# Optimization experiments

Hardware: AMD Instinct MI355X
Metric: run time of the kernel (lower is better)

Reference implementation:

```python
import jax, jax.numpy as jnp
import numpy as np

EPS = 1e-5
PDIM, QKD, DIM = 64, 16, 256
SCALE = QKD ** -0.5


def setup_inputs() -> dict:
    key = jax.random.key(0)
    ks = jax.random.split(key, 13)
    B, H, W = 8, 64, 64
    return {
        "x": jax.random.normal(ks[0], (B, DIM, H, W), jnp.float32),
        "gn_g": jax.random.uniform(ks[1], (PDIM,), jnp.float32, 0.5, 1.5),
        "gn_b": jax.random.normal(ks[2], (PDIM,), jnp.float32) * 0.1,
        "qkv_w": jax.random.normal(ks[3], (2 * QKD + PDIM, PDIM), jnp.float32) * (PDIM ** -0.5),
        "qkv_bn_g": jax.random.uniform(ks[4], (2 * QKD + PDIM,), jnp.float32, 0.5, 1.5),
        "qkv_bn_b": jax.random.normal(ks[5], (2 * QKD + PDIM,), jnp.float32) * 0.1,
        "qkv_rm": jax.random.normal(ks[6], (2 * QKD + PDIM,), jnp.float32) * 0.1,
        "qkv_rv": jax.random.uniform(ks[7], (2 * QKD + PDIM,), jnp.float32, 0.5, 1.5),
        "proj_w": jax.random.normal(ks[8], (DIM, DIM), jnp.float32) * (DIM ** -0.5),
        "proj_bn_g": jax.random.uniform(ks[9], (DIM,), jnp.float32, 0.5, 1.5),
        "proj_bn_b": jax.random.normal(ks[10], (DIM,), jnp.float32) * 0.1,
        "proj_rm": jax.random.normal(ks[11], (DIM,), jnp.float32) * 0.1,
        "proj_rv": jax.random.uniform(ks[12], (DIM,), jnp.float32, 0.5, 1.5),
    }


def _bn(y, g, b, rm, rv):
    # inference BatchNorm over channel axis 1 of [B,C,H,W]
    inv = g / jnp.sqrt(rv + EPS)
    return y * inv[None, :, None, None] + (b - rm * inv)[None, :, None, None]


def reference(x, gn_g, gn_b, qkv_w, qkv_bn_g, qkv_bn_b, qkv_rm, qkv_rv,
              proj_w, proj_bn_g, proj_bn_b, proj_rm, proj_rv):
    B, C, H, W = x.shape
    x1, x2 = x[:, :PDIM], x[:, PDIM:]
    # GroupNorm with 1 group: normalize over (C,H,W) per sample
    mu = jnp.mean(x1, axis=(1, 2, 3), keepdims=True)
    var = jnp.var(x1, axis=(1, 2, 3), keepdims=True)
    x1n = (x1 - mu) / jnp.sqrt(var + EPS)
    x1n = x1n * gn_g[None, :, None, None] + gn_b[None, :, None, None]
    # qkv: 1x1 conv + BN
    qkv = jnp.einsum('bchw,oc->bohw', x1n, qkv_w)
    qkv = _bn(qkv, qkv_bn_g, qkv_bn_b, qkv_rm, qkv_rv)
    q, k, v = qkv[:, :QKD], qkv[:, QKD:2 * QKD], qkv[:, 2 * QKD:]
    N = H * W
    q = q.reshape(B, QKD, N)
    k = k.reshape(B, QKD, N)
    v = v.reshape(B, PDIM, N)
    attn = jnp.einsum('bcn,bcm->bnm', q, k) * SCALE  # [B,N,N]
    attn = jax.nn.softmax(attn, axis=-1)
    x1_attn = jnp.einsum('bcm,bnm->bcn', v, attn).reshape(B, PDIM, H, W)
    xc = jnp.concatenate([x1_attn, x2], axis=1)
    # proj: ReLU -> 1x1 conv -> BN
    y = jnp.einsum('bchw,oc->bohw', jax.nn.relu(xc), proj_w)
    return _bn(y, proj_bn_g, proj_bn_b, proj_rm, proj_rv)
```

## Files before the change

### kernel.cpp

```cpp
#include <hip/hip_runtime.h>
#include <hip/hip_bf16.h>

typedef __bf16 bf16;
typedef __bf16 bf16x4 __attribute__((ext_vector_type(4)));
typedef __bf16 bf16x8 __attribute__((ext_vector_type(8)));
typedef float  f32x16 __attribute__((ext_vector_type(16)));

#define MFMA32 __builtin_amdgcn_mfma_f32_32x32x16_bf16
#define EPSV 1e-5f
#define QSCALE 0.36067376022224085f

__device__ __forceinline__ f32x16 fzero16() {
  f32x16 z;
#pragma unroll
  for (int i = 0; i < 16; ++i) z[i] = 0.f;
  return z;
}

__global__ __launch_bounds__(256) void k_stats_partial(const float* __restrict__ x,
                                                       float* __restrict__ part) {
  const int b = blockIdx.x >> 5, k = blockIdx.x & 31;
  const float* p = x + (size_t)b * 256 * 4096 + k * 8192;
  const int t = threadIdx.x;
  float s = 0.f, q = 0.f;
#pragma unroll
  for (int j = 0; j < 8; ++j) {
    float4 v = ((const float4*)p)[t + j * 256];
    s += v.x + v.y + v.z + v.w;
    q += v.x * v.x + v.y * v.y + v.z * v.z + v.w * v.w;
  }
  __shared__ float ls[256], lq[256];
  ls[t] = s; lq[t] = q;
  __syncthreads();
  for (int off = 128; off > 0; off >>= 1) {
    if (t < off) { ls[t] += ls[t + off]; lq[t] += lq[t + off]; }
    __syncthreads();
  }
  if (t == 0) { part[blockIdx.x * 2] = ls[0]; part[blockIdx.x * 2 + 1] = lq[0]; }
}

__global__ __launch_bounds__(256) void k_stats_final(const float* __restrict__ part,
                                                     float* __restrict__ stats) {
  const int t = threadIdx.x, b = t >> 5, k = t & 31;
  float s = part[(b * 32 + k) * 2], q = part[(b * 32 + k) * 2 + 1];
  for (int off = 16; off > 0; off >>= 1) {
    s += __shfl_down(s, off, 32);
    q += __shfl_down(q, off, 32);
  }
  if (k == 0) {
    const float inv_n = 1.f / 262144.f;
    const float mu = s * inv_n;
    const float var = q * inv_n - mu * mu;
    stats[b * 2] = mu;
    stats[b * 2 + 1] = rsqrtf(var + EPSV);
  }
}

__global__ __launch_bounds__(256) void k_qkv(
    const float* __restrict__ x, const float* __restrict__ gn_g, const float* __restrict__ gn_b,
    const float* __restrict__ qkv_w, const float* __restrict__ bn_g, const float* __restrict__ bn_b,
    const float* __restrict__ bn_rm, const float* __restrict__ bn_rv,
    const float* __restrict__ stats,
    bf16* __restrict__ qw, bf16* __restrict__ kw, bf16* __restrict__ vw) {
  const int b = blockIdx.x >> 6, tile = blockIdx.x & 63;
  const int n0 = tile * 64, t = threadIdx.x;
  __shared__ float xn[64][68];
  __shared__ float W[64][96];
  __shared__ float beta_s[96];
  const float mu = stats[b * 2], rstd = stats[b * 2 + 1];
  {
    const int c = t >> 2, f = t & 3;
    const float A = rstd * gn_g[c], B = gn_b[c] - mu * A;
    const float* xr = x + ((size_t)b * 256 + c) * 4096 + n0;
#pragma unroll
    for (int j = 0; j < 4; ++j) {
      float4 v = ((const float4*)xr)[f * 4 + j];
      const int nb = f * 16 + j * 4;
      xn[c][nb + 0] = v.x * A + B; xn[c][nb + 1] = v.y * A + B;
      xn[c][nb + 2] = v.z * A + B; xn[c][nb + 3] = v.w * A + B;
    }
  }
  for (int oc = t; oc < 96 * 8; oc += 256) {
    const int o = oc >> 3, ch = (oc & 7) * 8;
    const float inv = bn_g[o] * rsqrtf(bn_rv[o] + EPSV);
    if (ch == 0) beta_s[o] = bn_b[o] - bn_rm[o] * inv;
    const float* wr = qkv_w + o * 64 + ch;
#pragma unroll
    for (int i = 0; i < 8; ++i) W[ch + i][o] = wr[i] * inv;
  }
  __syncthreads();
  const int o_l = t & 31, ng = t >> 5;
#pragma unroll 1
  for (int p = 0; p < 3; ++p) {
    const int o = p * 32 + o_l;
    float acc[8];
#pragma unroll
    for (int j = 0; j < 8; ++j) acc[j] = 0.f;
    for (int c = 0; c < 64; ++c) {
      const float wv = W[c][o];
      const float* xr = &xn[c][ng * 8];
#pragma unroll
      for (int j = 0; j < 8; ++j) acc[j] += wv * xr[j];
    }
    const float beta = beta_s[o];
    const int nb = n0 + ng * 8;
    if (p == 0) {
      if (o < 16) {
#pragma unroll
        for (int j = 0; j < 8; ++j)
          qw[((size_t)b * 4096 + nb + j) * 16 + o] = (bf16)((acc[j] + beta) * QSCALE);
      } else {
#pragma unroll
        for (int j = 0; j < 8; ++j)
          kw[((size_t)b * 4096 + nb + j) * 16 + (o - 16)] = (bf16)(acc[j] + beta);
      }
    } else {
      const int c = (p - 1) * 32 + o_l;
      bf16* vr = vw + ((size_t)b * 64 + c) * 4096 + nb;
#pragma unroll
      for (int q4 = 0; q4 < 2; ++q4) {
        bf16x4 pk;
        pk[0] = (bf16)(acc[q4 * 4 + 0] + beta); pk[1] = (bf16)(acc[q4 * 4 + 1] + beta);
        pk[2] = (bf16)(acc[q4 * 4 + 2] + beta); pk[3] = (bf16)(acc[q4 * 4 + 3] + beta);
        *(bf16x4*)(vr + q4 * 4) = pk;
      }
    }
  }
}

__global__ __launch_bounds__(256) void k_prep_x2(const float* __restrict__ x,
                                                 bf16* __restrict__ xc) {
  const int b = blockIdx.x >> 5, nt = blockIdx.x & 31;
  const int n0 = nt * 128, t = threadIdx.x;
  __shared__ unsigned tile_u[128 * 100];
  const float* xb = x + ((size_t)b * 256 + 64) * 4096 + n0;
#pragma unroll
  for (int i = 0; i < 12; ++i) {
    const int idx = i * 256 + t;
    const int cp = idx >> 5, f = idx & 31;
    const float4 a = *(const float4*)(xb + (size_t)(2 * cp) * 4096 + f * 4);
    const float4 c4 = *(const float4*)(xb + (size_t)(2 * cp + 1) * 4096 + f * 4);
    const float av[4] = {a.x, a.y, a.z, a.w};
    const float cv[4] = {c4.x, c4.y, c4.z, c4.w};
#pragma unroll
    for (int e = 0; e < 4; ++e) {
      const int n = f * 4 + e;
      const unsigned u =
          (unsigned)__builtin_bit_cast(unsigned short, (bf16)fmaxf(av[e], 0.f)) |
          ((unsigned)__builtin_bit_cast(unsigned short, (bf16)fmaxf(cv[e], 0.f)) << 16);
      tile_u[n * 100 + cp] = u;
    }
  }
  __syncthreads();
#pragma unroll
  for (int i = 0; i < 12; ++i) {
    const int idx = i * 256 + t;
    const int n = idx / 24, q = idx % 24;
    const uint4 d = *(const uint4*)&tile_u[n * 100 + q * 4];
    *(uint4*)(xc + ((size_t)b * 4096 + n0 + n) * 256 + 64 + q * 8) = d;
  }
}

template<int SPLIT>
__global__ __launch_bounds__(256, 2) void k_attn_flash(
    const bf16* __restrict__ qw, const bf16* __restrict__ kw,
    const bf16* __restrict__ vw, bf16* __restrict__ xc,
    float* __restrict__ pl, bf16* __restrict__ pO) {
  constexpr int NT = 4096 / SPLIT / 64;
  constexpr int NBLK = SPLIT * 128;
  const int orig = blockIdx.x;
  const int wg = (orig & 7) * (NBLK / 8) + (orig >> 3);
  const int s = wg >> 7, b = (wg >> 4) & 7, qt = wg & 15;
  const int t = threadIdx.x, w = t >> 6, l = t & 63, ln = l & 31, g = l >> 5;

  __shared__ __align__(16) char kmem[2][2048];
  __shared__ __align__(16) char vmem[2][8192];

  const bf16* qb = qw + (size_t)b * 4096 * 16;
  const char* kb = (const char*)(kw + (size_t)b * 4096 * 16);
  const bf16* vb = vw + (size_t)b * 64 * 4096;
  const int m_start = s * (4096 / SPLIT);

  const char* ksrc = kb + (size_t)m_start * 32 + t * 8;
  const int klds = (((t >> 1) & 1) << 10) + ((t >> 2) << 4) + ((t & 1) << 3);
  const int vc = t >> 2, vq = t & 3;
  const bf16* vsrc = vb + (size_t)vc * 4096 + m_start + vq * 16;
  const int vswz = (vc & 15) * 8;

  const int nqbase = qt * 256 + w * 64 + ln;
  const bf16x8 qf0 = *(const bf16x8*)(qb + (size_t)nqbase * 16 + g * 8);
  const bf16x8 qf1 = *(const bf16x8*)(qb + (size_t)(nqbase + 32) * 16 + g * 8);

  uint2 kr = *(const uint2*)ksrc;
  uint4 vr0 = *(const uint4*)vsrc;
  uint4 vr1 = *(const uint4*)(vsrc + 8);
  *(uint2*)(kmem[0] + klds) = kr;
  {
    char* vrow = vmem[0] + vc * 128;
    *(uint2*)(vrow + ((vq * 32 +  0) ^ vswz)) = make_uint2(vr0.x, vr0.y);
    *(uint2*)(vrow + ((vq * 32 +  8) ^ vswz)) = make_uint2(vr0.z, vr0.w);
    *(uint2*)(vrow + ((vq * 32 + 16) ^ vswz)) = make_uint2(vr1.x, vr1.y);
    *(uint2*)(vrow + ((vq * 32 + 24) ^ vswz)) = make_uint2(vr1.z, vr1.w);
  }
  __syncthreads();

  f32x16 O00 = fzero16(), O01 = fzero16();
  f32x16 O10 = fzero16(), O11 = fzero16();
  float l0 = 0.f, l1 = 0.f;
  const int vsw = (ln & 15) * 8;

  int p = 0;
#pragma unroll 1
  for (int it = 0; it < NT; ++it) {
    if (it + 1 < NT) {
      kr  = *(const uint2*)(ksrc + (size_t)(it + 1) * 2048);
      vr0 = *(const uint4*)(vsrc + (it + 1) * 64);
      vr1 = *(const uint4*)(vsrc + (it + 1) * 64 + 8);
    }
    const bf16x8 kf0 = *(const bf16x8*)(kmem[p] + g * 1024 + ln * 16);
    const bf16x8 kf1 = *(const bf16x8*)(kmem[p] + g * 1024 + (ln + 32) * 16);
    bf16x8 pa0, pa1, pa2, pa3;
    {
      f32x16 S0 = MFMA32(kf0, qf0, fzero16(), 0, 0, 0);
      f32x16 S1 = MFMA32(kf1, qf0, fzero16(), 0, 0, 0);
      float ts = 0.f;
#pragma unroll
      for (int r = 0; r < 16; ++r) { S0[r] = __builtin_amdgcn_exp2f(S0[r]); ts += S0[r]; }
#pragma unroll
      for (int r = 0; r < 16; ++r) { S1[r] = __builtin_amdgcn_exp2f(S1[r]); ts += S1[r]; }
      ts += __shfl_xor(ts, 32, 64);
      l0 += ts;
#pragma unroll
      for (int r = 0; r < 8; ++r) {
        pa0[r] = (bf16)S0[r]; pa1[r] = (bf16)S0[r + 8];
        pa2[r] = (bf16)S1[r]; pa3[r] = (bf16)S1[r + 8];
      }
    }
    bf16x8 pc0, pc1, pc2, pc3;
    {
      f32x16 S0 = MFMA32(kf0, qf1, fzero16(), 0, 0, 0);
      f32x16 S1 = MFMA32(kf1, qf1, fzero16(), 0, 0, 0);
      float ts = 0.f;
#pragma unroll
      for (int r = 0; r < 16; ++r) { S0[r] = __builtin_amdgcn_exp2f(S0[r]); ts += S0[r]; }
#pragma unroll
      for (int r = 0; r < 16; ++r) { S1[r] = __builtin_amdgcn_exp2f(S1[r]); ts += S1[r]; }
      ts += __shfl_xor(ts, 32, 64);
      l1 += ts;
#pragma unroll
      for (int r = 0; r < 8; ++r) {
        pc0[r] = (bf16)S0[r]; pc1[r] = (bf16)S0[r + 8];
        pc2[r] = (bf16)S1[r]; pc3[r] = (bf16)S1[r + 8];
      }
    }
    {
      const char* rlo = vmem[p] + ln * 128;
      const char* rhi = vmem[p] + (ln + 32) * 128;
#pragma unroll
      for (int kg = 0; kg < 4; ++kg) {
        const int c0 = (kg * 32 + 8 * g) ^ vsw;
        const int c1 = (kg * 32 + 16 + 8 * g) ^ vsw;
        bf16x4 lo = *(const bf16x4*)(rlo + c0);
        bf16x4 hi = *(const bf16x4*)(rlo + c1);
        const bf16x8 va0 = __builtin_shufflevector(lo, hi, 0, 1, 2, 3, 4, 5, 6, 7);
        lo = *(const bf16x4*)(rhi + c0);
        hi = *(const bf16x4*)(rhi + c1);
        const bf16x8 va1 = __builtin_shufflevector(lo, hi, 0, 1, 2, 3, 4, 5, 6, 7);
        const bf16x8 pa = kg == 0 ? pa0 : kg == 1 ? pa1 : kg == 2 ? pa2 : pa3;
        const bf16x8 pc = kg == 0 ? pc0 : kg == 1 ? pc1 : kg == 2 ? pc2 : pc3;
        O00 = MFMA32(va0, pa, O00, 0, 0, 0);
        O01 = MFMA32(va1, pa, O01, 0, 0, 0);
        O10 = MFMA32(va0, pc, O10, 0, 0, 0);
        O11 = MFMA32(va1, pc, O11, 0, 0, 0);
      }
    }
    if (it + 1 < NT) {
      *(uint2*)(kmem[p ^ 1] + klds) = kr;
      char* vrow = vmem[p ^ 1] + vc * 128;
      *(uint2*)(vrow + ((vq * 32 +  0) ^ vswz)) = make_uint2(vr0.x, vr0.y);
      *(uint2*)(vrow + ((vq * 32 +  8) ^ vswz)) = make_uint2(vr0.z, vr0.w);
      *(uint2*)(vrow + ((vq * 32 + 16) ^ vswz)) = make_uint2(vr1.x, vr1.y);
      *(uint2*)(vrow + ((vq * 32 + 24) ^ vswz)) = make_uint2(vr1.z, vr1.w);
    }
    __syncthreads();
    p ^= 1;
  }

  if constexpr (SPLIT > 1) {
    const size_t sbase = (size_t)(s * 8 + b) * 4096 + qt * 256 + w * 64;
#pragma unroll
    for (int h = 0; h < 2; ++h) {
      const f32x16& Oc0 = h ? O10 : O00;
      const f32x16& Oc1 = h ? O11 : O01;
      const size_t n_idx = sbase + h * 32 + ln;
      bf16* row = pO + n_idx * 64;
#pragma unroll
      for (int q4 = 0; q4 < 4; ++q4) {
        bf16x4 e0, e1;
#pragma unroll
        for (int i = 0; i < 4; ++i) {
          e0[i] = (bf16)Oc0[q4 * 4 + i];
          e1[i] = (bf16)Oc1[q4 * 4 + i];
        }
        *(bf16x4*)(row + q4 * 8 + 4 * g) = e0;
        *(bf16x4*)(row + 32 + q4 * 8 + 4 * g) = e1;
      }
      if (g == 0) pl[n_idx] = h ? l1 : l0;
    }
  } else {
    const size_t nb = (size_t)b * 4096 + qt * 256 + w * 64;
#pragma unroll
    for (int h = 0; h < 2; ++h) {
      const f32x16& Oc0 = h ? O10 : O00;
      const f32x16& Oc1 = h ? O11 : O01;
      const float rl = 1.0f / (h ? l1 : l0);
      bf16* row = xc + (nb + h * 32 + ln) * 256;
#pragma unroll
      for (int q4 = 0; q4 < 4; ++q4) {
        bf16x4 e0, e1;
#pragma unroll
        for (int i = 0; i < 4; ++i) {
          e0[i] = (bf16)fmaxf(Oc0[q4 * 4 + i] * rl, 0.f);
          e1[i] = (bf16)fmaxf(Oc1[q4 * 4 + i] * rl, 0.f);
        }
        *(bf16x4*)(row + q4 * 8 + 4 * g) = e0;
        *(bf16x4*)(row + 32 + q4 * 8 + 4 * g) = e1;
      }
    }
  }
}

template<int SPLIT>
__global__ __launch_bounds__(256) void k_attn_combine(
    const float* __restrict__ pl, const bf16* __restrict__ pO,
    bf16* __restrict__ xc) {
  const int b = blockIdx.x >> 5, ht = blockIdx.x & 31;
  const int t = threadIdx.x;
  const int n = ht * 128 + (t & 127), ch = (t >> 7) * 32;
  float L = 0.f;
#pragma unroll
  for (int s = 0; s < SPLIT; ++s)
    L += pl[(size_t)(s * 8 + b) * 4096 + n];
  const float rL = 1.0f / L;
  float acc[32];
#pragma unroll
  for (int j = 0; j < 32; ++j) acc[j] = 0.f;
#pragma unroll
  for (int s = 0; s < SPLIT; ++s) {
    const bf16* row = pO + ((size_t)(s * 8 + b) * 4096 + n) * 64 + ch;
#pragma unroll
    for (int u = 0; u < 4; ++u) {
      const bf16x8 v = *(const bf16x8*)(row + u * 8);
#pragma unroll
      for (int e = 0; e < 8; ++e) acc[u * 8 + e] += (float)v[e];
    }
  }
  bf16* dst = xc + ((size_t)b * 4096 + n) * 256 + ch;
#pragma unroll
  for (int u = 0; u < 4; ++u) {
    bf16x8 o8;
#pragma unroll
    for (int e = 0; e < 8; ++e) o8[e] = (bf16)fmaxf(acc[u * 8 + e] * rL, 0.f);
    *(bf16x8*)(dst + u * 8) = o8;
  }
}

__global__ __launch_bounds__(256, 2) void k_proj(
    const bf16* __restrict__ xc, const float* __restrict__ pw,
    const float* __restrict__ bn_g, const float* __restrict__ bn_b,
    const float* __restrict__ bn_rm, const float* __restrict__ bn_rv,
    float* __restrict__ out) {
  const int orig = blockIdx.x;
  const int wg = (orig & 7) * 64 + (orig >> 3);
  const int b = wg >> 6, rem = wg & 63, nt = rem >> 1, oh = rem & 1;
  const int n0 = nt * 128, o0 = oh * 128;
  const int t = threadIdx.x, w = t >> 6, l = t & 63, ln = l & 31, g = l >> 5;

  __shared__ __align__(16) bf16 pws[128 * 256];
  __shared__ float beta_s[128];

  {
    const int o = t >> 1, half = t & 1;
    const float inv = bn_g[o0 + o] * rsqrtf(bn_rv[o0 + o] + EPSV);
    if (half == 0) beta_s[o] = bn_b[o0 + o] - bn_rm[o0 + o] * inv;
    const float* wr = pw + (size_t)(o0 + o) * 256 + half * 128;
    const int s_hh = (o & 15) * 8;
#pragma unroll
    for (int j = 0; j < 16; ++j) {
      const float4 a = ((const float4*)wr)[j * 2];
      const float4 c4 = ((const float4*)wr)[j * 2 + 1];
      bf16x8 v8;
      v8[0] = (bf16)(a.x * inv);  v8[1] = (bf16)(a.y * inv);
      v8[2] = (bf16)(a.z * inv);  v8[3] = (bf16)(a.w * inv);
      v8[4] = (bf16)(c4.x * inv); v8[5] = (bf16)(c4.y * inv);
      v8[6] = (bf16)(c4.z * inv); v8[7] = (bf16)(c4.w * inv);
      *(bf16x8*)&pws[o * 256 + ((half * 128 + j * 8) ^ s_hh)] = v8;
    }
  }
  __syncthreads();

  const bf16* xrow = xc + ((size_t)b * 4096 + n0 + w * 32 + ln) * 256;
  const int sw = (ln & 15) * 8;
  f32x16 acc0 = fzero16(), acc1 = fzero16(), acc2 = fzero16(), acc3 = fzero16();
#pragma unroll 4
  for (int ck = 0; ck < 256; ck += 16) {
    const bf16x8 bfrag = *(const bf16x8*)(xrow + ck + g * 8);
    const int cidx = (ck + g * 8) ^ sw;
    const bf16x8 a0 = *(const bf16x8*)&pws[(ln) * 256 + cidx];
    const bf16x8 a1 = *(const bf16x8*)&pws[(32 + ln) * 256 + cidx];
    const bf16x8 a2 = *(const bf16x8*)&pws[(64 + ln) * 256 + cidx];
    const bf16x8 a3 = *(const bf16x8*)&pws[(96 + ln) * 256 + cidx];
    acc0 = MFMA32(a0, bfrag, acc0, 0, 0, 0);
    acc1 = MFMA32(a1, bfrag, acc1, 0, 0, 0);
    acc2 = MFMA32(a2, bfrag, acc2, 0, 0, 0);
    acc3 = MFMA32(a3, bfrag, acc3, 0, 0, 0);
  }
  const int ncol = n0 + w * 32 + ln;
  float* ob = out + (size_t)b * 256 * 4096 + ncol;
#pragma unroll
  for (int og = 0; og < 4; ++og) {
    const f32x16& A = og == 0 ? acc0 : og == 1 ? acc1 : og == 2 ? acc2 : acc3;
#pragma unroll
    for (int r = 0; r < 16; ++r) {
      const int o_loc = og * 32 + (r & 3) + 8 * (r >> 2) + 4 * g;
      ob[(size_t)(o0 + o_loc) * 4096] = A[r] + beta_s[o_loc];
    }
  }
}

extern "C" void kernel_launch(void* const* d_in, const int* in_sizes, int n_in,
                              void* d_out, int out_size, void* d_ws, size_t ws_size,
                              hipStream_t stream) {
  (void)in_sizes; (void)n_in; (void)out_size;
  const float* x        = (const float*)d_in[0];
  const float* gn_g     = (const float*)d_in[1];
  const float* gn_b     = (const float*)d_in[2];
  const float* qkv_w    = (const float*)d_in[3];
  const float* qkv_bn_g = (const float*)d_in[4];
  const float* qkv_bn_b = (const float*)d_in[5];
  const float* qkv_rm   = (const float*)d_in[6];
  const float* qkv_rv   = (const float*)d_in[7];
  const float* proj_w   = (const float*)d_in[8];
  const float* proj_bn_g = (const float*)d_in[9];
  const float* proj_bn_b = (const float*)d_in[10];
  const float* proj_rm  = (const float*)d_in[11];
  const float* proj_rv  = (const float*)d_in[12];

  char* ws = (char*)d_ws;
  float* part  = (float*)ws;
  float* stats = (float*)(ws + 4096);
  bf16* qw = (bf16*)(ws + 8192);
  bf16* kw = (bf16*)(ws + 8192 + (1u << 20));
  bf16* vw = (bf16*)(ws + 8192 + (2u << 20));
  bf16* xc = (bf16*)(ws + 8192 + (6u << 20));

  const size_t base = 8192 + (22u << 20);
  const size_t npq = (size_t)8 * 4096;
  const size_t need2 = base + 2 * npq * (4 + 64 * 2);
  const size_t need4 = base + 4 * npq * (4 + 64 * 2);
  const int split = (ws_size >= need4) ? 4 : (ws_size >= need2) ? 2 : 1;

  k_stats_partial<<<256, 256, 0, stream>>>(x, part);
  k_stats_final<<<1, 256, 0, stream>>>(part, stats);
  k_qkv<<<512, 256, 0, stream>>>(x, gn_g, gn_b, qkv_w, qkv_bn_g, qkv_bn_b,
                                 qkv_rm, qkv_rv, stats, qw, kw, vw);
  k_prep_x2<<<256, 256, 0, stream>>>(x, xc);

  if (split == 4) {
    float* pl = (float*)(ws + base);
    bf16* pO = (bf16*)(ws + base + 4 * npq * 4);
    k_attn_flash<4><<<512, 256, 0, stream>>>(qw, kw, vw, xc, pl, pO);
    k_attn_combine<4><<<256, 256, 0, stream>>>(pl, pO, xc);
  } else if (split == 2) {
    float* pl = (float*)(ws + base);
    bf16* pO = (bf16*)(ws + base + 2 * npq * 4);
    k_attn_flash<2><<<256, 256, 0, stream>>>(qw, kw, vw, xc, pl, pO);
    k_attn_combine<2><<<256, 256, 0, stream>>>(pl, pO, xc);
  } else {
    k_attn_flash<1><<<128, 256, 0, stream>>>(qw, kw, vw, xc, nullptr, nullptr);
  }

  k_proj<<<512, 256, 0, stream>>>(xc, proj_w, proj_bn_g, proj_bn_b,
                                  proj_rm, proj_rv, (float*)d_out);
}
```

Measured before the change: 100.2 us.

## Fuse split-KV attention, combine and x2 prep into one 1024-thread kernel

Replaces the separate split-KV flash kernel, global-memory combine kernel and x2 relu/transpose kernel with one kernel. Each 1024-thread block covers 128 queries, and its four 256-thread groups each process a quarter of the keys. The partial sums are reduced through shared memory instead of global scratch, and the same block then writes the relu'd x2 half of xc. This removes two launches and the partial-output round trip through global memory. In exchange each wave now handles 32 queries instead of 64, which halves K/V reuse per wave, and the block uses 80KB of shared memory, which limits occupancy.

```diff
diff --git a/kernel.cpp b/kernel.cpp
--- a/kernel.cpp
+++ b/kernel.cpp
@@ -128,75 +128,40 @@
   }
 }
 
-__global__ __launch_bounds__(256) void k_prep_x2(const float* __restrict__ x,
-                                                 bf16* __restrict__ xc) {
-  const int b = blockIdx.x >> 5, nt = blockIdx.x & 31;
-  const int n0 = nt * 128, t = threadIdx.x;
-  __shared__ unsigned tile_u[128 * 100];
-  const float* xb = x + ((size_t)b * 256 + 64) * 4096 + n0;
-#pragma unroll
-  for (int i = 0; i < 12; ++i) {
-    const int idx = i * 256 + t;
-    const int cp = idx >> 5, f = idx & 31;
-    const float4 a = *(const float4*)(xb + (size_t)(2 * cp) * 4096 + f * 4);
-    const float4 c4 = *(const float4*)(xb + (size_t)(2 * cp + 1) * 4096 + f * 4);
-    const float av[4] = {a.x, a.y, a.z, a.w};
-    const float cv[4] = {c4.x, c4.y, c4.z, c4.w};
-#pragma unroll
-    for (int e = 0; e < 4; ++e) {
-      const int n = f * 4 + e;
-      const unsigned u =
-          (unsigned)__builtin_bit_cast(unsigned short, (bf16)fmaxf(av[e], 0.f)) |
-          ((unsigned)__builtin_bit_cast(unsigned short, (bf16)fmaxf(cv[e], 0.f)) << 16);
-      tile_u[n * 100 + cp] = u;
-    }
-  }
-  __syncthreads();
-#pragma unroll
-  for (int i = 0; i < 12; ++i) {
-    const int idx = i * 256 + t;
-    const int n = idx / 24, q = idx % 24;
-    const uint4 d = *(const uint4*)&tile_u[n * 100 + q * 4];
-    *(uint4*)(xc + ((size_t)b * 4096 + n0 + n) * 256 + 64 + q * 8) = d;
-  }
-}
-
-template<int SPLIT>
-__global__ __launch_bounds__(256, 2) void k_attn_flash(
+__global__ __launch_bounds__(1024, 4) void k_attn(
     const bf16* __restrict__ qw, const bf16* __restrict__ kw,
-    const bf16* __restrict__ vw, bf16* __restrict__ xc,
-    float* __restrict__ pl, bf16* __restrict__ pO) {
-  constexpr int NT = 4096 / SPLIT / 64;
-  constexpr int NBLK = SPLIT * 128;
+    const bf16* __restrict__ vw, const float* __restrict__ x,
+    bf16* __restrict__ xc) {
+  __shared__ __align__(16) char smem[81920];
   const int orig = blockIdx.x;
-  const int wg = (orig & 7) * (NBLK / 8) + (orig >> 3);
-  const int s = wg >> 7, b = (wg >> 4) & 7, qt = wg & 15;
-  const int t = threadIdx.x, w = t >> 6, l = t & 63, ln = l & 31, g = l >> 5;
-
-  __shared__ __align__(16) char kmem[2][2048];
-  __shared__ __align__(16) char vmem[2][8192];
+  const int wg = (orig & 7) * 32 + (orig >> 3);
+  const int b = wg >> 5, qt = wg & 31;
+  const int t = threadIdx.x;
+  const int grp = t >> 8, tg = t & 255;
+  const int wv4 = tg >> 6, l = t & 63, ln = l & 31, g = l >> 5;
 
   const bf16* qb = qw + (size_t)b * 4096 * 16;
   const char* kb = (const char*)(kw + (size_t)b * 4096 * 16);
   const bf16* vb = vw + (size_t)b * 64 * 4096;
-  const int m_start = s * (4096 / SPLIT);
-
-  const char* ksrc = kb + (size_t)m_start * 32 + t * 8;
-  const int klds = (((t >> 1) & 1) << 10) + ((t >> 2) << 4) + ((t & 1) << 3);
-  const int vc = t >> 2, vq = t & 3;
-  const bf16* vsrc = vb + (size_t)vc * 4096 + m_start + vq * 16;
+  const int m0 = grp * 1024;
+
+  char* kbase = smem + grp * 4096;
+  char* vbase = smem + 16384 + grp * 16384;
+
+  const char* ksrc = kb + (size_t)m0 * 32 + tg * 8;
+  const int klds = (((tg >> 1) & 1) << 10) + ((tg >> 2) << 4) + ((tg & 1) << 3);
+  const int vc = tg >> 2, vq = tg & 3;
+  const bf16* vsrc = vb + (size_t)vc * 4096 + m0 + vq * 16;
   const int vswz = (vc & 15) * 8;
 
-  const int nqbase = qt * 256 + w * 64 + ln;
-  const bf16x8 qf0 = *(const bf16x8*)(qb + (size_t)nqbase * 16 + g * 8);
-  const bf16x8 qf1 = *(const bf16x8*)(qb + (size_t)(nqbase + 32) * 16 + g * 8);
+  const bf16x8 qf = *(const bf16x8*)(qb + (size_t)(qt * 128 + wv4 * 32 + ln) * 16 + g * 8);
 
   uint2 kr = *(const uint2*)ksrc;
   uint4 vr0 = *(const uint4*)vsrc;
   uint4 vr1 = *(const uint4*)(vsrc + 8);
-  *(uint2*)(kmem[0] + klds) = kr;
-  {
-    char* vrow = vmem[0] + vc * 128;
+  *(uint2*)(kbase + klds) = kr;
+  {
+    char* vrow = vbase + vc * 128;
     *(uint2*)(vrow + ((vq * 32 +  0) ^ vswz)) = make_uint2(vr0.x, vr0.y);
     *(uint2*)(vrow + ((vq * 32 +  8) ^ vswz)) = make_uint2(vr0.z, vr0.w);
     *(uint2*)(vrow + ((vq * 32 + 16) ^ vswz)) = make_uint2(vr1.x, vr1.y);
@@ -204,79 +169,56 @@
   }
   __syncthreads();
 
-  f32x16 O00 = fzero16(), O01 = fzero16();
-  f32x16 O10 = fzero16(), O11 = fzero16();
-  float l0 = 0.f, l1 = 0.f;
+  f32x16 O0 = fzero16(), O1 = fzero16();
+  float l_run = 0.f;
   const int vsw = (ln & 15) * 8;
 
   int p = 0;
 #pragma unroll 1
-  for (int it = 0; it < NT; ++it) {
-    if (it + 1 < NT) {
+  for (int it = 0; it < 16; ++it) {
+    if (it + 1 < 16) {
       kr  = *(const uint2*)(ksrc + (size_t)(it + 1) * 2048);
       vr0 = *(const uint4*)(vsrc + (it + 1) * 64);
       vr1 = *(const uint4*)(vsrc + (it + 1) * 64 + 8);
     }
-    const bf16x8 kf0 = *(const bf16x8*)(kmem[p] + g * 1024 + ln * 16);
-    const bf16x8 kf1 = *(const bf16x8*)(kmem[p] + g * 1024 + (ln + 32) * 16);
-    bf16x8 pa0, pa1, pa2, pa3;
+    const bf16x8 kf0 = *(const bf16x8*)(kbase + p * 2048 + g * 1024 + ln * 16);
+    const bf16x8 kf1 = *(const bf16x8*)(kbase + p * 2048 + g * 1024 + (ln + 32) * 16);
+    f32x16 S0 = MFMA32(kf0, qf, fzero16(), 0, 0, 0);
+    f32x16 S1 = MFMA32(kf1, qf, fzero16(), 0, 0, 0);
+    float ts = 0.f;
+#pragma unroll
+    for (int r = 0; r < 16; ++r) { S0[r] = __builtin_amdgcn_exp2f(S0[r]); ts += S0[r]; }
+#pragma unroll
+    for (int r = 0; r < 16; ++r) { S1[r] = __builtin_amdgcn_exp2f(S1[r]); ts += S1[r]; }
+    ts += __shfl_xor(ts, 32, 64);
+    l_run += ts;
+    bf16x8 pb0, pb1, pb2, pb3;
+#pragma unroll
+    for (int r = 0; r < 8; ++r) {
+      pb0[r] = (bf16)S0[r]; pb1[r] = (bf16)S0[r + 8];
+      pb2[r] = (bf16)S1[r]; pb3[r] = (bf16)S1[r + 8];
+    }
     {
-      f32x16 S0 = MFMA32(kf0, qf0, fzero16(), 0, 0, 0);
-      f32x16 S1 = MFMA32(kf1, qf0, fzero16(), 0, 0, 0);
-      float ts = 0.f;
-#pragma unroll
-      for (int r = 0; r < 16; ++r) { S0[r] = __builtin_amdgcn_exp2f(S0[r]); ts += S0[r]; }
-#pragma unroll
-      for (int r = 0; r < 16; ++r) { S1[r] = __builtin_amdgcn_exp2f(S1[r]); ts += S1[r]; }
-      ts += __shfl_xor(ts, 32, 64);
-      l0 += ts;
-#pragma unroll
-      for (int r = 0; r < 8; ++r) {
-        pa0[r] = (bf16)S0[r]; pa1[r] = (bf16)S0[r + 8];
-        pa2[r] = (bf16)S1[r]; pa3[r] = (bf16)S1[r + 8];
-      }
-    }
-    bf16x8 pc0, pc1, pc2, pc3;
-    {
-      f32x16 S0 = MFMA32(kf0, qf1, fzero16(), 0, 0, 0);
-      f32x16 S1 = MFMA32(kf1, qf1, fzero16(), 0, 0, 0);
-      float ts = 0.f;
-#pragma unroll
-      for (int r = 0; r < 16; ++r) { S0[r] = __builtin_amdgcn_exp2f(S0[r]); ts += S0[r]; }
-#pragma unroll
-      for (int r = 0; r < 16; ++r) { S1[r] = __builtin_amdgcn_exp2f(S1[r]); ts += S1[r]; }
-      ts += __shfl_xor(ts, 32, 64);
-      l1 += ts;
-#pragma unroll
-      for (int r = 0; r < 8; ++r) {
-        pc0[r] = (bf16)S0[r]; pc1[r] = (bf16)S0[r + 8];
-        pc2[r] = (bf16)S1[r]; pc3[r] = (bf16)S1[r + 8];
-      }
-    }
-    {
-      const char* rlo = vmem[p] + ln * 128;
-      const char* rhi = vmem[p] + (ln + 32) * 128;
+      const char* rlo = vbase + p * 8192 + ln * 128;
+      const char* rhi = vbase + p * 8192 + (ln + 32) * 128;
 #pragma unroll
       for (int kg = 0; kg < 4; ++kg) {
         const int c0 = (kg * 32 + 8 * g) ^ vsw;
         const int c1 = (kg * 32 + 16 + 8 * g) ^ vsw;
         bf16x4 lo = *(const bf16x4*)(rlo + c0);
         bf16x4 hi = *(const bf16x4*)(rlo + c1);
-        const bf16x8 va0 = __builtin_shufflevector(lo, hi, 0, 1, 2, 3, 4, 5, 6, 7);
+        bf16x8 va = __builtin_shufflevector(lo, hi, 0, 1, 2, 3, 4, 5, 6, 7);
+        const bf16x8 pb = kg == 0 ? pb0 : kg == 1 ? pb1 : kg == 2 ? pb2 : pb3;
+        O0 = MFMA32(va, pb, O0, 0, 0, 0);
         lo = *(const bf16x4*)(rhi + c0);
         hi = *(const bf16x4*)(rhi + c1);
-        const bf16x8 va1 = __builtin_shufflevector(lo, hi, 0, 1, 2, 3, 4, 5, 6, 7);
-        const bf16x8 pa = kg == 0 ? pa0 : kg == 1 ? pa1 : kg == 2 ? pa2 : pa3;
-        const bf16x8 pc = kg == 0 ? pc0 : kg == 1 ? pc1 : kg == 2 ? pc2 : pc3;
-        O00 = MFMA32(va0, pa, O00, 0, 0, 0);
-        O01 = MFMA32(va1, pa, O01, 0, 0, 0);
-        O10 = MFMA32(va0, pc, O10, 0, 0, 0);
-        O11 = MFMA32(va1, pc, O11, 0, 0, 0);
-      }
-    }
-    if (it + 1 < NT) {
-      *(uint2*)(kmem[p ^ 1] + klds) = kr;
-      char* vrow = vmem[p ^ 1] + vc * 128;
+        va = __builtin_shufflevector(lo, hi, 0, 1, 2, 3, 4, 5, 6, 7);
+        O1 = MFMA32(va, pb, O1, 0, 0, 0);
+      }
+    }
+    if (it + 1 < 16) {
+      *(uint2*)(kbase + (p ^ 1) * 2048 + klds) = kr;
+      char* vrow = vbase + (p ^ 1) * 8192 + vc * 128;
       *(uint2*)(vrow + ((vq * 32 +  0) ^ vswz)) = make_uint2(vr0.x, vr0.y);
       *(uint2*)(vrow + ((vq * 32 +  8) ^ vswz)) = make_uint2(vr0.z, vr0.w);
       *(uint2*)(vrow + ((vq * 32 + 16) ^ vswz)) = make_uint2(vr1.x, vr1.y);
@@ -286,82 +228,74 @@
     p ^= 1;
   }
 
-  if constexpr (SPLIT > 1) {
-    const size_t sbase = (size_t)(s * 8 + b) * 4096 + qt * 256 + w * 64;
+  {
+    const int nl = wv4 * 32 + ln;
+    char* orow = smem + 16384 + grp * 16384 + nl * 128;
+    const int xr = (nl & 7) << 4;
 #pragma unroll
     for (int h = 0; h < 2; ++h) {
-      const f32x16& Oc0 = h ? O10 : O00;
-      const f32x16& Oc1 = h ? O11 : O01;
-      const size_t n_idx = sbase + h * 32 + ln;
-      bf16* row = pO + n_idx * 64;
+      const f32x16& O = h ? O1 : O0;
 #pragma unroll
       for (int q4 = 0; q4 < 4; ++q4) {
-        bf16x4 e0, e1;
-#pragma unroll
-        for (int i = 0; i < 4; ++i) {
-          e0[i] = (bf16)Oc0[q4 * 4 + i];
-          e1[i] = (bf16)Oc1[q4 * 4 + i];
-        }
-        *(bf16x4*)(row + q4 * 8 + 4 * g) = e0;
-        *(bf16x4*)(row + 32 + q4 * 8 + 4 * g) = e1;
-      }
-      if (g == 0) pl[n_idx] = h ? l1 : l0;
-    }
-  } else {
-    const size_t nb = (size_t)b * 4096 + qt * 256 + w * 64;
-#pragma unroll
-    for (int h = 0; h < 2; ++h) {
-      const f32x16& Oc0 = h ? O10 : O00;
-      const f32x16& Oc1 = h ? O11 : O01;
-      const float rl = 1.0f / (h ? l1 : l0);
-      bf16* row = xc + (nb + h * 32 + ln) * 256;
-#pragma unroll
-      for (int q4 = 0; q4 < 4; ++q4) {
-        bf16x4 e0, e1;
-#pragma unroll
-        for (int i = 0; i < 4; ++i) {
-          e0[i] = (bf16)fmaxf(Oc0[q4 * 4 + i] * rl, 0.f);
-          e1[i] = (bf16)fmaxf(Oc1[q4 * 4 + i] * rl, 0.f);
-        }
-        *(bf16x4*)(row + q4 * 8 + 4 * g) = e0;
-        *(bf16x4*)(row + 32 + q4 * 8 + 4 * g) = e1;
-      }
-    }
-  }
-}
-
-template<int SPLIT>
-__global__ __launch_bounds__(256) void k_attn_combine(
-    const float* __restrict__ pl, const bf16* __restrict__ pO,
-    bf16* __restrict__ xc) {
-  const int b = blockIdx.x >> 5, ht = blockIdx.x & 31;
-  const int t = threadIdx.x;
-  const int n = ht * 128 + (t & 127), ch = (t >> 7) * 32;
-  float L = 0.f;
-#pragma unroll
-  for (int s = 0; s < SPLIT; ++s)
-    L += pl[(size_t)(s * 8 + b) * 4096 + n];
-  const float rL = 1.0f / L;
-  float acc[32];
-#pragma unroll
-  for (int j = 0; j < 32; ++j) acc[j] = 0.f;
-#pragma unroll
-  for (int s = 0; s < SPLIT; ++s) {
-    const bf16* row = pO + ((size_t)(s * 8 + b) * 4096 + n) * 64 + ch;
-#pragma unroll
-    for (int u = 0; u < 4; ++u) {
-      const bf16x8 v = *(const bf16x8*)(row + u * 8);
-#pragma unroll
-      for (int e = 0; e < 8; ++e) acc[u * 8 + e] += (float)v[e];
-    }
-  }
-  bf16* dst = xc + ((size_t)b * 4096 + n) * 256 + ch;
-#pragma unroll
-  for (int u = 0; u < 4; ++u) {
-    bf16x8 o8;
-#pragma unroll
-    for (int e = 0; e < 8; ++e) o8[e] = (bf16)fmaxf(acc[u * 8 + e] * rL, 0.f);
-    *(bf16x8*)(dst + u * 8) = o8;
+        bf16x4 e;
+#pragma unroll
+        for (int i = 0; i < 4; ++i) e[i] = (bf16)O[q4 * 4 + i];
+        *(bf16x4*)(orow + ((h * 64 + q4 * 16 + g * 8) ^ xr)) = e;
+      }
+    }
+    if (g == 0) *(float*)(smem + grp * 4096 + nl * 4) = l_run;
+  }
+  __syncthreads();
+  {
+    const int n8 = t >> 3, o8 = t & 7;
+    const int xr = (n8 & 7) << 4;
+    float L = 0.f;
+    float acc[8];
+#pragma unroll
+    for (int e = 0; e < 8; ++e) acc[e] = 0.f;
+#pragma unroll
+    for (int gr = 0; gr < 4; ++gr) {
+      L += *(const float*)(smem + gr * 4096 + n8 * 4);
+      const bf16x8 v = *(const bf16x8*)(smem + 16384 + gr * 16384 + n8 * 128 +
+                                        ((o8 * 16) ^ xr));
+#pragma unroll
+      for (int e = 0; e < 8; ++e) acc[e] += (float)v[e];
+    }
+    const float rL = 1.0f / L;
+    bf16x8 o;
+#pragma unroll
+    for (int e = 0; e < 8; ++e) o[e] = (bf16)fmaxf(acc[e] * rL, 0.f);
+    *(bf16x8*)(xc + ((size_t)b * 4096 + qt * 128 + n8) * 256 + o8 * 8) = o;
+  }
+  __syncthreads();
+
+  {
+    unsigned* tile_u = (unsigned*)smem;
+    const float* xb = x + ((size_t)b * 256 + 64) * 4096 + qt * 128;
+#pragma unroll
+    for (int i = 0; i < 3; ++i) {
+      const int idx = i * 1024 + t;
+      const int cp = idx >> 5, f = idx & 31;
+      const float4 a = *(const float4*)(xb + (size_t)(2 * cp) * 4096 + f * 4);
+      const float4 c4 = *(const float4*)(xb + (size_t)(2 * cp + 1) * 4096 + f * 4);
+      const float av[4] = {a.x, a.y, a.z, a.w};
+      const float cv[4] = {c4.x, c4.y, c4.z, c4.w};
+#pragma unroll
+      for (int e = 0; e < 4; ++e) {
+        const unsigned u =
+            (unsigned)__builtin_bit_cast(unsigned short, (bf16)fmaxf(av[e], 0.f)) |
+            ((unsigned)__builtin_bit_cast(unsigned short, (bf16)fmaxf(cv[e], 0.f)) << 16);
+        tile_u[(f * 4 + e) * 100 + cp] = u;
+      }
+    }
+    __syncthreads();
+#pragma unroll
+    for (int i = 0; i < 3; ++i) {
+      const int idx = i * 1024 + t;
+      const int n = idx / 24, q = idx % 24;
+      const uint4 d = *(const uint4*)&tile_u[n * 100 + q * 4];
+      *(uint4*)(xc + ((size_t)b * 4096 + qt * 128 + n) * 256 + 64 + q * 8) = d;
+    }
   }
 }
 
@@ -431,7 +365,7 @@
 extern "C" void kernel_launch(void* const* d_in, const int* in_sizes, int n_in,
                               void* d_out, int out_size, void* d_ws, size_t ws_size,
                               hipStream_t stream) {
-  (void)in_sizes; (void)n_in; (void)out_size;
+  (void)in_sizes; (void)n_in; (void)out_size; (void)ws_size;
   const float* x        = (const float*)d_in[0];
   const float* gn_g     = (const float*)d_in[1];
   const float* gn_b     = (const float*)d_in[2];
@@ -454,32 +388,11 @@
   bf16* vw = (bf16*)(ws + 8192 + (2u << 20));
   bf16* xc = (bf16*)(ws + 8192 + (6u << 20));
 
-  const size_t base = 8192 + (22u << 20);
-  const size_t npq = (size_t)8 * 4096;
-  const size_t need2 = base + 2 * npq * (4 + 64 * 2);
-  const size_t need4 = base + 4 * npq * (4 + 64 * 2);
-  const int split = (ws_size >= need4) ? 4 : (ws_size >= need2) ? 2 : 1;
-
   k_stats_partial<<<256, 256, 0, stream>>>(x, part);
   k_stats_final<<<1, 256, 0, stream>>>(part, stats);
   k_qkv<<<512, 256, 0, stream>>>(x, gn_g, gn_b, qkv_w, qkv_bn_g, qkv_bn_b,
                                  qkv_rm, qkv_rv, stats, qw, kw, vw);
-  k_prep_x2<<<256, 256, 0, stream>>>(x, xc);
-
-  if (split == 4) {
-    float* pl = (float*)(ws + base);
-    bf16* pO = (bf16*)(ws + base + 4 * npq * 4);
-    k_attn_flash<4><<<512, 256, 0, stream>>>(qw, kw, vw, xc, pl, pO);
-    k_attn_combine<4><<<256, 256, 0, stream>>>(pl, pO, xc);
-  } else if (split == 2) {
-    float* pl = (float*)(ws + base);
-    bf16* pO = (bf16*)(ws + base + 2 * npq * 4);
-    k_attn_flash<2><<<256, 256, 0, stream>>>(qw, kw, vw, xc, pl, pO);
-    k_attn_combine<2><<<256, 256, 0, stream>>>(pl, pO, xc);
-  } else {
-    k_attn_flash<1><<<128, 256, 0, stream>>>(qw, kw, vw, xc, nullptr, nullptr);
-  }
-
+  k_attn<<<256, 1024, 0, stream>>>(qw, kw, vw, x, xc);
   k_proj<<<512, 256, 0, stream>>>(xc, proj_w, proj_bn_g, proj_bn_b,
                                   proj_rm, proj_rv, (float*)d_out);
 }
```

New measurement: 90.62 us. 1.11x faster.
